# Kernel optimization log

Hardware: AMD Instinct MI355X
Metric: run time of the kernel (lower is better)

Reference implementation:

```python
import jax, jax.numpy as jnp
import numpy as np

EPS = 1e-5  # BatchNorm1d eps


def _glorot(key, shape):
    fan_in, fan_out = shape[0], shape[1]
    lim = float(np.sqrt(6.0 / (fan_in + fan_out)))
    return jax.random.uniform(key, shape, jnp.float32, -lim, lim)


def setup_inputs() -> dict:
    key = jax.random.key(0)
    ks = jax.random.split(key, 6)
    N, IN, H, OUT = 50000, 128, 64, 64
    E = 800000
    x = jax.random.normal(ks[0], (N, IN), jnp.float32)
    edge_index = jax.random.randint(ks[1], (2, E), 0, N, jnp.int64)
    return {
        "x": x,
        "edge_index": edge_index,
        "W1": _glorot(ks[2], (IN, H)),
        "b1": jnp.zeros((H,), jnp.float32),
        "gamma1": jnp.ones((H,), jnp.float32),
        "beta1": jnp.zeros((H,), jnp.float32),
        "W2": _glorot(ks[3], (H, OUT)),
        "b2": jnp.zeros((OUT,), jnp.float32),
        "gamma2": jnp.ones((OUT,), jnp.float32),
        "beta2": jnp.zeros((OUT,), jnp.float32),
    }


def _gcn_conv(x, W, b, src, dst, norm, n):
    # x' = D^{-1/2} (A + I) D^{-1/2} X W + b  (PyG GCNConv, edge_weight=None)
    h = x @ W                              # [N, F]
    msg = h[src] * norm[:, None]           # gather + scale, [E+N, F]
    out = jax.ops.segment_sum(msg, dst, num_segments=n)  # scatter-add
    return out + b


def _batch_norm(h, gamma, beta):
    # training-mode BN over node dim, biased variance (as torch uses for normalization)
    mean = h.mean(0)
    var = h.var(0)
    return (h - mean) * jax.lax.rsqrt(var + EPS) * gamma + beta


def reference(x, edge_index, W1, b1, gamma1, beta1, W2, b2, gamma2, beta2):
    n = x.shape[0]
    # add self loops
    loop = jnp.arange(n, dtype=edge_index.dtype)
    src = jnp.concatenate([edge_index[0], loop])
    dst = jnp.concatenate([edge_index[1], loop])
    # symmetric degree normalization (deg >= 1 thanks to self loops)
    deg = jax.ops.segment_sum(jnp.ones(src.shape[0], x.dtype), dst, num_segments=n)
    dinv = jax.lax.rsqrt(jnp.maximum(deg, 1e-12))
    norm = dinv[src] * dinv[dst]           # [E+N]

    # layer 1: GCNConv -> BN -> ReLU (dropout = identity in eval)
    h = _gcn_conv(x, W1, b1, src, dst, norm, n)
    h = jax.nn.relu(_batch_norm(h, gamma1, beta1))
    # layer 2: GCNConv -> BN (no activation on last layer)
    h = _gcn_conv(h, W2, b2, src, dst, norm, n)
    h = _batch_norm(h, gamma2, beta2)
    return h
```

## Files before the change

### kernel.cpp

```cpp
#include <hip/hip_runtime.h>
#include <hip/hip_fp16.h>
#include <math.h>

#define EPS 1e-5f
#define CAP 64

__global__ void k_zero(int* __restrict__ cnt, float* __restrict__ stats,
                       __half* __restrict__ Ylo, __half* __restrict__ Yhi, int N) {
    int i = blockIdx.x * blockDim.x + threadIdx.x;
    if (i < N) cnt[i] = 0;
    if (i < 256) stats[i] = 0.0f;
    if (i < 16) {
        ((int*)(Ylo + (size_t)N * 32))[i] = 0;
        ((int*)(Yhi + (size_t)N * 32))[i] = 0;
    }
}

__global__ void k_dinv(const int* __restrict__ cnt, float* __restrict__ dinv, int N) {
    int i = blockIdx.x * blockDim.x + threadIdx.x;
    if (i < N) dinv[i] = rsqrtf((float)(cnt[i] + 1));
    if (i == 0) dinv[N] = 0.0f;
}

__global__ void k_scale(__half2* __restrict__ Ylo2, __half2* __restrict__ Yhi2,
                        const float* __restrict__ dinv, int N) {
    int i = blockIdx.x * blockDim.x + threadIdx.x;
    if (i < N * 16) {
        float d = dinv[i >> 4];
        float2 a = __half22float2(Ylo2[i]);
        a.x *= d; a.y *= d;
        Ylo2[i] = __float22half2_rn(a);
        float2 b = __half22float2(Yhi2[i]);
        b.x *= d; b.y *= d;
        Yhi2[i] = __float22half2_rn(b);
    }
}

__global__ __launch_bounds__(256) void k_gemm1_fill(const float* __restrict__ x,
                                                    const float* __restrict__ W1,
                                                    __half* __restrict__ Ylo,
                                                    __half* __restrict__ Yhi, int N,
                                                    const int* __restrict__ src,
                                                    const int* __restrict__ dst,
                                                    int* __restrict__ cnt,
                                                    unsigned short* __restrict__ csr,
                                                    int E, int G) {
    if ((int)blockIdx.x >= G) {
        int t = (blockIdx.x - G) * 256 + threadIdx.x;
        int stride = (gridDim.x - G) * 256;
        for (int e = t; e < E; e += stride) {
            int d = dst[e];
            int pos = atomicAdd(&cnt[d], 1);
            if (pos < CAP)
                __builtin_nontemporal_store((unsigned short)src[e], &csr[(size_t)d * CAP + pos]);
        }
        return;
    }
    __shared__ float w[128 * 64];
    __shared__ float xs[4][4][128];
    for (int i = threadIdx.x; i < 128 * 64; i += 256) w[i] = W1[i];
    __syncthreads();
    int lane = threadIdx.x & 63;
    int wave = threadIdx.x >> 6;
    int half = lane >> 5, l = lane & 31;
    __half* Yout = half ? Yhi : Ylo;
    int gwave = blockIdx.x * 4 + wave;
    int nw = G * 4;
    for (int r0 = gwave * 4; r0 < N; r0 += nw * 4) {
        int nr = min(4, N - r0);
        for (int j = 0; j < nr; ++j) {
            xs[wave][j][lane]      = x[(size_t)(r0 + j) * 128 + lane];
            xs[wave][j][64 + lane] = x[(size_t)(r0 + j) * 128 + 64 + lane];
        }
        float a0 = 0.f, a1 = 0.f, a2 = 0.f, a3 = 0.f;
#pragma unroll 8
        for (int k = 0; k < 128; ++k) {
            float wk = w[k * 64 + lane];
            a0 += xs[wave][0][k] * wk;
            a1 += xs[wave][1][k] * wk;
            a2 += xs[wave][2][k] * wk;
            a3 += xs[wave][3][k] * wk;
        }
        Yout[(size_t)(r0 + 0) * 32 + l] = __float2half(a0);
        if (nr > 1) Yout[(size_t)(r0 + 1) * 32 + l] = __float2half(a1);
        if (nr > 2) Yout[(size_t)(r0 + 2) * 32 + l] = __float2half(a2);
        if (nr > 3) Yout[(size_t)(r0 + 3) * 32 + l] = __float2half(a3);
    }
}

__global__ __launch_bounds__(256) void k_agg(const __half* __restrict__ Ylo,
                                             const __half* __restrict__ Yhi,
                                             const unsigned short* __restrict__ csr,
                                             const int* __restrict__ cnt,
                                             const float* __restrict__ dinv,
                                             float* __restrict__ H,
                                             float* __restrict__ stats, int N) {
    __shared__ float lbuf[4][32];
    __shared__ float ssum[4][32], ssq[4][32];
    int half = blockIdx.x & 1;
    const __half* Y = half ? Yhi : Ylo;
    int lane = threadIdx.x & 63;
    int wave = threadIdx.x >> 6;
    int g = lane >> 2;
    int c4 = lane & 3;
    int slot = (blockIdx.x >> 1) * 4 + wave;
    int nslots = (gridDim.x >> 1) * 4;
    float s = 0.f, q = 0.f;
    for (int v = slot; v < N; v += nslots) {
        int c = min(cnt[v], CAP);
        float dv = dinv[v];
        int ent = (int)csr[(size_t)v * CAP + lane];
        float acc[8];
        {
            int4 yv = *(const int4*)(Y + (size_t)v * 32 + c4 * 8);
            const __half2* hp = (const __half2*)&yv;
            float selfw = (g == 0) ? 1.f : 0.f;
#pragma unroll
            for (int k = 0; k < 4; ++k) {
                float2 p = __half22float2(hp[k]);
                acc[2 * k]     = selfw * p.x;
                acc[2 * k + 1] = selfw * p.y;
            }
        }
        int nb = (c + 15) >> 4;
        for (int b = 0; b < nb; ++b) {
            int idx = __shfl(ent, b * 16 + g, 64);
            idx = min(idx, N);
            int4 yv = *(const int4*)(Y + (size_t)idx * 32 + c4 * 8);
            const __half2* hp = (const __half2*)&yv;
#pragma unroll
            for (int k = 0; k < 4; ++k) {
                float2 p = __half22float2(hp[k]);
                acc[2 * k]     += p.x;
                acc[2 * k + 1] += p.y;
            }
        }
#pragma unroll
        for (int m = 4; m <= 32; m <<= 1)
#pragma unroll
            for (int k = 0; k < 8; ++k) acc[k] += __shfl_xor(acc[k], m, 64);
        if (g == 0) {
#pragma unroll
            for (int k = 0; k < 8; ++k) lbuf[wave][c4 * 8 + k] = acc[k] * dv;
        }
        if (lane < 32) {
            float h = lbuf[wave][lane];
            __builtin_nontemporal_store(h, &H[(size_t)v * 64 + half * 32 + lane]);
            s += h; q += h * h;
        }
    }
    if (lane < 32) { ssum[wave][lane] = s; ssq[wave][lane] = q; }
    __syncthreads();
    if (threadIdx.x < 32) {
        float ts = ssum[0][threadIdx.x] + ssum[1][threadIdx.x] + ssum[2][threadIdx.x] + ssum[3][threadIdx.x];
        float tq = ssq[0][threadIdx.x] + ssq[1][threadIdx.x] + ssq[2][threadIdx.x] + ssq[3][threadIdx.x];
        atomicAdd(&stats[half * 32 + threadIdx.x], ts);
        atomicAdd(&stats[64 + half * 32 + threadIdx.x], tq);
    }
}

__global__ __launch_bounds__(256) void k_gemm2(const float* __restrict__ H1,
                                               const float* __restrict__ stats,
                                               const float* __restrict__ gamma,
                                               const float* __restrict__ beta,
                                               const float* __restrict__ W2,
                                               const float* __restrict__ dinv,
                                               __half* __restrict__ Ylo,
                                               __half* __restrict__ Yhi, int N) {
    __shared__ float w[64 * 64];
    __shared__ float xs[4][4][64];
    for (int i = threadIdx.x; i < 64 * 64; i += 256) w[i] = W2[i];
    int lane = threadIdx.x & 63;
    int wave = threadIdx.x >> 6;
    int half = lane >> 5, l = lane & 31;
    __half* Yout = half ? Yhi : Ylo;
    float mean = stats[lane] / (float)N;
    float var = stats[64 + lane] / (float)N - mean * mean;
    float rstd = rsqrtf(var + EPS);
    float g = gamma[lane], bt = beta[lane];
    __syncthreads();
    int gwave = blockIdx.x * 4 + wave;
    int nw = gridDim.x * 4;
    for (int r0 = gwave * 4; r0 < N; r0 += nw * 4) {
        int nr = min(4, N - r0);
        for (int j = 0; j < nr; ++j) {
            float v = H1[(size_t)(r0 + j) * 64 + lane];
            v = (v - mean) * rstd * g + bt;
            xs[wave][j][lane] = fmaxf(v, 0.f);
        }
        float a0 = 0.f, a1 = 0.f, a2 = 0.f, a3 = 0.f;
#pragma unroll 8
        for (int k = 0; k < 64; ++k) {
            float wk = w[k * 64 + lane];
            a0 += xs[wave][0][k] * wk;
            a1 += xs[wave][1][k] * wk;
            a2 += xs[wave][2][k] * wk;
            a3 += xs[wave][3][k] * wk;
        }
        Yout[(size_t)(r0 + 0) * 32 + l] = __float2half(a0 * dinv[r0]);
        if (nr > 1) Yout[(size_t)(r0 + 1) * 32 + l] = __float2half(a1 * dinv[r0 + 1]);
        if (nr > 2) Yout[(size_t)(r0 + 2) * 32 + l] = __float2half(a2 * dinv[r0 + 2]);
        if (nr > 3) Yout[(size_t)(r0 + 3) * 32 + l] = __float2half(a3 * dinv[r0 + 3]);
    }
}

__global__ void k_bnfinal(float* __restrict__ out, const float* __restrict__ stats,
                          const float* __restrict__ gamma, const float* __restrict__ beta,
                          int N) {
    int i = blockIdx.x * blockDim.x + threadIdx.x;
    int total = N * 64;
    if (i < total) {
        int f = i & 63;
        float mean = stats[f] / (float)N;
        float var = stats[64 + f] / (float)N - mean * mean;
        float rstd = rsqrtf(var + EPS);
        out[i] = (out[i] - mean) * rstd * gamma[f] + beta[f];
    }
}

extern "C" void kernel_launch(void* const* d_in, const int* in_sizes, int n_in,
                              void* d_out, int out_size, void* d_ws, size_t ws_size,
                              hipStream_t stream) {
    const float* x      = (const float*)d_in[0];
    const int*   ei     = (const int*)d_in[1];
    const float* W1     = (const float*)d_in[2];
    const float* gamma1 = (const float*)d_in[4];
    const float* beta1  = (const float*)d_in[5];
    const float* W2     = (const float*)d_in[6];
    const float* gamma2 = (const float*)d_in[8];
    const float* beta2  = (const float*)d_in[9];
    float* out = (float*)d_out;

    const int N = in_sizes[0] / 128;
    const int E = in_sizes[1] / 2;
    const int* src = ei;
    const int* dst = ei + E;

    char* ws = (char*)d_ws;
    int*   cnt   = (int*)  ws;
    float* stats = (float*)(ws + 0x40000);
    float* dinv  = (float*)(ws + 0x50000);
    __half* Ylo  = (__half*)(ws + 0x90000);
    __half* Yhi  = (__half*)(ws + 0x90000 + 0x320000);
    float* H1    = (float*)(ws + 0x90000 + 0x640000);
    unsigned short* csr = (unsigned short*)(ws + 0x90000 + 0x640000 + 0xC40000);

    const int B = (N + 255) / 256;
    const int total = N * 64;
    const int G = 640, F = 384;

    k_zero<<<B, 256, 0, stream>>>(cnt, stats, Ylo, Yhi, N);
    hipMemsetAsync(csr, 0xFF, (size_t)N * CAP * 2, stream);

    k_gemm1_fill<<<G + F, 256, 0, stream>>>(x, W1, Ylo, Yhi, N, src, dst, cnt, csr, E, G);
    k_dinv<<<B, 256, 0, stream>>>(cnt, dinv, N);
    k_scale<<<(N * 16 + 255) / 256, 256, 0, stream>>>((__half2*)Ylo, (__half2*)Yhi, dinv, N);
    k_agg<<<2048, 256, 0, stream>>>(Ylo, Yhi, csr, cnt, dinv, H1, stats, N);

    k_gemm2<<<1024, 256, 0, stream>>>(H1, stats, gamma1, beta1, W2, dinv, Ylo, Yhi, N);
    k_agg<<<2048, 256, 0, stream>>>(Ylo, Yhi, csr, cnt, dinv, out, stats + 128, N);
    k_bnfinal<<<(total + 255) / 256, 256, 0, stream>>>(out, stats + 128, gamma2, beta2, N);
}
```

Baseline: 283.1 us.

## Fold source scaling into aggregation, fuse CSR init, partition edge fill into teams

Removes the separate k_scale pass by multiplying each gathered neighbor row by its dinv inside the first aggregation (templated PRESCALED flag). The hipMemset of the CSR buffer moves into the init kernel as vectorized int4 stores. The edge-fill blocks now split into 8 teams that each handle only destinations with matching low bits, which raises locality of the atomics but makes every team read the whole edge list. The aggregation grid is doubled, and the stores become regular instead of nontemporal.

```diff
diff --git a/kernel.cpp b/kernel.cpp
--- a/kernel.cpp
+++ b/kernel.cpp
@@ -5,10 +5,16 @@
 #define EPS 1e-5f
 #define CAP 64
 
-__global__ void k_zero(int* __restrict__ cnt, float* __restrict__ stats,
-                       __half* __restrict__ Ylo, __half* __restrict__ Yhi, int N) {
+__global__ void k_init(int* __restrict__ cnt, float* __restrict__ stats,
+                       __half* __restrict__ Ylo, __half* __restrict__ Yhi,
+                       unsigned short* __restrict__ csr, int N) {
     int i = blockIdx.x * blockDim.x + threadIdx.x;
-    if (i < N) cnt[i] = 0;
+    if (i < N) {
+        cnt[i] = 0;
+        int4* p = (int4*)(csr + (size_t)i * CAP);
+#pragma unroll
+        for (int k = 0; k < 8; ++k) p[k] = make_int4(-1, -1, -1, -1);
+    }
     if (i < 256) stats[i] = 0.0f;
     if (i < 16) {
         ((int*)(Ylo + (size_t)N * 32))[i] = 0;
@@ -20,20 +26,6 @@
     int i = blockIdx.x * blockDim.x + threadIdx.x;
     if (i < N) dinv[i] = rsqrtf((float)(cnt[i] + 1));
     if (i == 0) dinv[N] = 0.0f;
-}
-
-__global__ void k_scale(__half2* __restrict__ Ylo2, __half2* __restrict__ Yhi2,
-                        const float* __restrict__ dinv, int N) {
-    int i = blockIdx.x * blockDim.x + threadIdx.x;
-    if (i < N * 16) {
-        float d = dinv[i >> 4];
-        float2 a = __half22float2(Ylo2[i]);
-        a.x *= d; a.y *= d;
-        Ylo2[i] = __float22half2_rn(a);
-        float2 b = __half22float2(Yhi2[i]);
-        b.x *= d; b.y *= d;
-        Yhi2[i] = __float22half2_rn(b);
-    }
 }
 
 __global__ __launch_bounds__(256) void k_gemm1_fill(const float* __restrict__ x,
@@ -46,13 +38,15 @@
                                                     unsigned short* __restrict__ csr,
                                                     int E, int G) {
     if ((int)blockIdx.x >= G) {
-        int t = (blockIdx.x - G) * 256 + threadIdx.x;
-        int stride = (gridDim.x - G) * 256;
-        for (int e = t; e < E; e += stride) {
+        int team = blockIdx.x & 7;
+        int tb = (int)(blockIdx.x - G) >> 3;
+        int nb = (int)(gridDim.x - G) >> 3;
+        for (int e = tb * 256 + (int)threadIdx.x; e < E; e += nb * 256) {
             int d = dst[e];
-            int pos = atomicAdd(&cnt[d], 1);
-            if (pos < CAP)
-                __builtin_nontemporal_store((unsigned short)src[e], &csr[(size_t)d * CAP + pos]);
+            if ((d & 7) == team) {
+                int pos = atomicAdd(&cnt[d], 1);
+                if (pos < CAP) csr[(size_t)d * CAP + pos] = (unsigned short)src[e];
+            }
         }
         return;
     }
@@ -88,6 +82,7 @@
     }
 }
 
+template <bool PRESCALED>
 __global__ __launch_bounds__(256) void k_agg(const __half* __restrict__ Ylo,
                                              const __half* __restrict__ Yhi,
                                              const unsigned short* __restrict__ csr,
@@ -114,7 +109,7 @@
         {
             int4 yv = *(const int4*)(Y + (size_t)v * 32 + c4 * 8);
             const __half2* hp = (const __half2*)&yv;
-            float selfw = (g == 0) ? 1.f : 0.f;
+            float selfw = (g == 0) ? (PRESCALED ? 1.f : dv) : 0.f;
 #pragma unroll
             for (int k = 0; k < 4; ++k) {
                 float2 p = __half22float2(hp[k]);
@@ -126,13 +121,14 @@
         for (int b = 0; b < nb; ++b) {
             int idx = __shfl(ent, b * 16 + g, 64);
             idx = min(idx, N);
+            float de = PRESCALED ? 1.f : dinv[idx];
             int4 yv = *(const int4*)(Y + (size_t)idx * 32 + c4 * 8);
             const __half2* hp = (const __half2*)&yv;
 #pragma unroll
             for (int k = 0; k < 4; ++k) {
                 float2 p = __half22float2(hp[k]);
-                acc[2 * k]     += p.x;
-                acc[2 * k + 1] += p.y;
+                acc[2 * k]     += de * p.x;
+                acc[2 * k + 1] += de * p.y;
             }
         }
 #pragma unroll
@@ -249,15 +245,13 @@
     const int total = N * 64;
     const int G = 640, F = 384;
 
-    k_zero<<<B, 256, 0, stream>>>(cnt, stats, Ylo, Yhi, N);
-    hipMemsetAsync(csr, 0xFF, (size_t)N * CAP * 2, stream);
+    k_init<<<B, 256, 0, stream>>>(cnt, stats, Ylo, Yhi, csr, N);
 
     k_gemm1_fill<<<G + F, 256, 0, stream>>>(x, W1, Ylo, Yhi, N, src, dst, cnt, csr, E, G);
     k_dinv<<<B, 256, 0, stream>>>(cnt, dinv, N);
-    k_scale<<<(N * 16 + 255) / 256, 256, 0, stream>>>((__half2*)Ylo, (__half2*)Yhi, dinv, N);
-    k_agg<<<2048, 256, 0, stream>>>(Ylo, Yhi, csr, cnt, dinv, H1, stats, N);
+    k_agg<false><<<4096, 256, 0, stream>>>(Ylo, Yhi, csr, cnt, dinv, H1, stats, N);
 
     k_gemm2<<<1024, 256, 0, stream>>>(H1, stats, gamma1, beta1, W2, dinv, Ylo, Yhi, N);
-    k_agg<<<2048, 256, 0, stream>>>(Ylo, Yhi, csr, cnt, dinv, out, stats + 128, N);
+    k_agg<true><<<4096, 256, 0, stream>>>(Ylo, Yhi, csr, cnt, dinv, out, stats + 128, N);
     k_bnfinal<<<(total + 255) / 256, 256, 0, stream>>>(out, stats + 128, gamma2, beta2, N);
 }
```

Result: slower. 320.5 us (+13.2%).
